# Performance work log

Hardware: AMD Instinct MI355X
Metric: run time of the kernel (lower is better)

The kernel has to match this reference:

```python
import jax, jax.numpy as jnp
import numpy as np

EPS_RHO = 1e-8
EPS_DEN = 1e-9


def _rho_signed_sqrt(x):
    return jnp.sqrt(jax.nn.relu(x) + EPS_RHO) - jnp.sqrt(jax.nn.relu(-x) + EPS_RHO)


def setup_inputs() -> dict:
    key = jax.random.key(0)
    ks = jax.random.split(key, 8)
    B, N, C, A = 2, 512, 1024, 64  # batch, seq, hidden_dim, attn_dim
    s_c = 1.0 / np.sqrt(C)
    s_a = 1.0 / np.sqrt(A)
    return {
        "X": jax.random.normal(ks[0], (B, N, C), jnp.float32),
        "Wq": jax.random.normal(ks[1], (A, C), jnp.float32) * s_c,   # Linear(C->A), no bias
        "Wk": jax.random.normal(ks[2], (A, C), jnp.float32) * s_c,   # Linear(C->A), no bias
        "Wphi": jax.random.normal(ks[3], (A,), jnp.float32) * s_a,   # Linear(A->1), no bias
        "Wy_w": jax.random.normal(ks[4], (C, C), jnp.float32) * s_c, # Linear(C->C)
        "Wy_b": jax.random.normal(ks[5], (C,), jnp.float32) * s_c,
        "We_w": jax.random.normal(ks[6], (C, A), jnp.float32) * s_a, # Linear(A->C)
        "We_b": jax.random.normal(ks[7], (C,), jnp.float32) * s_a,
    }


def reference(X, Wq, Wk, Wphi, Wy_w, Wy_b, We_w, We_b):
    # q, k: (B,N,A); Vy: (B,N,C)
    q = jnp.einsum('bnc,ac->bna', X, Wq)
    k = jnp.einsum('bnc,ac->bna', X, Wk)
    Vy = jnp.einsum('bnc,dc->bnd', X, Wy_w) + Wy_b

    # pairwise features e_ij = relu(rho(q_i + k_j)): (B,N,N,A)
    e = jax.nn.relu(_rho_signed_sqrt(q[:, :, None, :] + k[:, None, :, :]))

    # scores: (B,N,N); stable exp with per-row max (== online-softmax result)
    scores = jnp.einsum('bija,a->bij', e, Wphi)
    m = jnp.max(scores, axis=-1, keepdims=True)
    ex = jnp.exp(scores - m)
    denom = jnp.sum(ex, axis=-1)  # (B,N)

    # part1 = exp_scores @ Vy
    part1 = jnp.einsum('bij,bjc->bic', ex, Vy)
    # part2 = sum_j ex_ij * (We e_ij + be) = We(sum_j ex_ij e_ij) + be * denom  (We is linear)
    Ew = jnp.einsum('bij,bija->bia', ex, e)  # (B,N,A)
    part2 = jnp.einsum('bia,ca->bic', Ew, We_w) + We_b * denom[..., None]

    return (part1 + part2) / (denom[..., None] + EPS_DEN)
```

## Files before the change

kernel.cpp:

```cpp
#include <hip/hip_runtime.h>
#include <math.h>

#define EPS_RHO 1e-8f
#define EPS_DEN 1e-9f

constexpr int Bb = 2;
constexpr int Nn = 512;
constexpr int Cc = 1024;
constexpr int Aa = 64;
constexpr int TOK = Bb * Nn;
constexpr int KGP = 576;

typedef __attribute__((ext_vector_type(8))) short short8;
typedef __attribute__((ext_vector_type(4))) short short4v;
typedef __attribute__((ext_vector_type(4))) float f32x4;

__device__ __forceinline__ float e_fn(float s) {
    const float SQE = 9.9999994e-05f;
    return sqrtf(fmaxf(s, 0.f) + EPS_RHO) - SQE;
}

__device__ __forceinline__ short f2bf(float x) {
    union { float f; unsigned u; } v; v.f = x;
    unsigned r = v.u + 0x7FFFu + ((v.u >> 16) & 1u);
    return (short)(r >> 16);
}

__device__ __forceinline__ unsigned cvt_pk_bf16(float e0, float e1) {
    unsigned d;
    asm("v_cvt_pk_bf16_f32 %0, %1, %2" : "=v"(d) : "v"(e0), "v"(e1));
    return d;
}

constexpr int PREP_N0 = 1024 * 1024;
constexpr int PREP_N1 = 1152 * 1024;
constexpr int PREP_N2 = 2 * 1024 * 64;
constexpr int PREP_TOT = PREP_N0 + PREP_N1 + PREP_N2;

__global__ __launch_bounds__(256) void prep_kernel(
    const float* __restrict__ X, const float* __restrict__ Wy_w,
    const float* __restrict__ Wq, const float* __restrict__ Wk,
    const float* __restrict__ We_w,
    short* __restrict__ Xb, short* __restrict__ Wb, short* __restrict__ Gt)
{
    int g = (blockIdx.x * 256 + threadIdx.x) * 4;
    if (g >= PREP_TOT) return;

    const float* src;
    short* dst;
    if (g < PREP_N0) {
        src = X + g;
        dst = Xb + g;
    } else if (g < PREP_N0 + PREP_N1) {
        int i2 = g - PREP_N0;
        if (i2 < 1048576)       src = Wy_w + i2;
        else if (i2 < 1114112)  src = Wq + (i2 - 1048576);
        else                    src = Wk + (i2 - 1114112);
        dst = Wb + i2;
    } else {
        int i3 = g - PREP_N0 - PREP_N1;
        int b = i3 >> 16;
        int r = i3 & 65535;
        int c = r >> 6, a = r & 63;
        src = We_w + (size_t)c * Aa + a;
        dst = Gt + ((size_t)(b * 1024 + c)) * KGP + 512 + a;
    }
    float4 v = *(const float4*)src;
    short4v o = { f2bf(v.x), f2bf(v.y), f2bf(v.z), f2bf(v.w) };
    *(short4v*)dst = o;
}

__global__ __launch_bounds__(256) void mega_gemm(
    const short* __restrict__ Xb,
    const short* __restrict__ Wb,
    const float* __restrict__ Wy_b,
    short* __restrict__ Gt,
    float* __restrict__ qg,
    float* __restrict__ kTg)
{
    constexpr int K = 1024, BK = 64;
    __shared__ short As[64][72];
    __shared__ short Bs[64][72];

    int tid = threadIdx.x;
    int bm = blockIdx.y * 64;
    int bn = blockIdx.x * 64;
    int row = tid >> 2;
    int kq  = (tid & 3) << 4;

    const short* ag = Xb + (size_t)(bm + row) * K + kq;
    const short* bg = Wb + (size_t)(bn + row) * K + kq;

    short8 ar[2], br[2];
    ar[0] = *(const short8*)ag;       ar[1] = *(const short8*)(ag + 8);
    br[0] = *(const short8*)bg;       br[1] = *(const short8*)(bg + 8);

    int wid = tid >> 6, lane = tid & 63;
    int wm = (wid & 1) * 32, wn = (wid >> 1) * 32;
    int fr = lane & 15, fk = (lane >> 4) * 8;

    f32x4 acc[2][2] = {};

    for (int step = 0; step < K / BK; ++step) {
        __syncthreads();
        *(short8*)&As[row][kq]     = ar[0];
        *(short8*)&As[row][kq + 8] = ar[1];
        *(short8*)&Bs[row][kq]     = br[0];
        *(short8*)&Bs[row][kq + 8] = br[1];
        __syncthreads();

        if (step + 1 < K / BK) {
            const short* ag2 = ag + (size_t)(step + 1) * BK;
            const short* bg2 = bg + (size_t)(step + 1) * BK;
            ar[0] = *(const short8*)ag2;  ar[1] = *(const short8*)(ag2 + 8);
            br[0] = *(const short8*)bg2;  br[1] = *(const short8*)(bg2 + 8);
        }

        #pragma unroll
        for (int kk = 0; kk < 2; ++kk) {
            short8 af[2], bfr[2];
            #pragma unroll
            for (int mi = 0; mi < 2; ++mi)
                af[mi] = *(const short8*)&As[wm + mi * 16 + fr][kk * 32 + fk];
            #pragma unroll
            for (int ni = 0; ni < 2; ++ni)
                bfr[ni] = *(const short8*)&Bs[wn + ni * 16 + fr][kk * 32 + fk];
            #pragma unroll
            for (int mi = 0; mi < 2; ++mi)
                #pragma unroll
                for (int ni = 0; ni < 2; ++ni)
                    acc[mi][ni] = __builtin_amdgcn_mfma_f32_16x16x32_bf16(
                        af[mi], bfr[ni], acc[mi][ni], 0, 0, 0);
        }
    }

    int cr = (lane >> 4) * 4;
    int cc = lane & 15;
    if (bn < 1024) {
        #pragma unroll
        for (int mi = 0; mi < 2; ++mi)
            #pragma unroll
            for (int ni = 0; ni < 2; ++ni) {
                int c = bn + wn + ni * 16 + cc;
                float bv = Wy_b[c];
                #pragma unroll
                for (int r_ = 0; r_ < 4; ++r_) {
                    int t = bm + wm + mi * 16 + cr + r_;
                    int b = t >> 9, j = t & 511;
                    Gt[((size_t)(b * 1024 + c)) * KGP + j] = f2bf(acc[mi][ni][r_] + bv);
                }
            }
    } else if (bn == 1024) {
        #pragma unroll
        for (int mi = 0; mi < 2; ++mi)
            #pragma unroll
            for (int ni = 0; ni < 2; ++ni) {
                int a = wn + ni * 16 + cc;
                #pragma unroll
                for (int r_ = 0; r_ < 4; ++r_) {
                    int t = bm + wm + mi * 16 + cr + r_;
                    qg[(size_t)t * Aa + a] = acc[mi][ni][r_];
                }
            }
    } else {
        #pragma unroll
        for (int mi = 0; mi < 2; ++mi)
            #pragma unroll
            for (int ni = 0; ni < 2; ++ni) {
                int a = wn + ni * 16 + cc;
                #pragma unroll
                for (int r_ = 0; r_ < 4; ++r_) {
                    int t = bm + wm + mi * 16 + cr + r_;
                    int b = t >> 9, j = t & 511;
                    kTg[((size_t)(b * 64 + a)) * 512 + j] = acc[mi][ni][r_];
                }
            }
    }
}

__global__ __launch_bounds__(256) void attn1_fused(
    const float* __restrict__ qg,
    const float* __restrict__ kTg,
    const float* __restrict__ Wphi,
    short* __restrict__ P,
    float* __restrict__ denomg)
{
    __shared__ __align__(16) float qs[Aa];
    __shared__ __align__(16) float wph[Aa];
    __shared__ __align__(16) short E[256][72];
    __shared__ __align__(16) float exs[256];
    __shared__ __align__(16) float red[256];
    __shared__ __align__(16) float ewp[8][Aa];

    int t = blockIdx.x;
    int b = t >> 9;
    int tid = threadIdx.x;

    if (tid < Aa) {
        qs[tid] = qg[(size_t)t * Aa + tid];
        wph[tid] = Wphi[tid];
    }
    __syncthreads();

    const float* kT = kTg + (size_t)b * Aa * 512;

    float dsum = 0.f;
    float ew0 = 0.f, ew1 = 0.f;
    int pa2 = (tid & 31) * 2;
    int pg8 = tid >> 5;

    #pragma unroll
    for (int c = 0; c < 2; ++c) {
        int j = c * 256 + tid;

        float s = 0.f;
        #pragma unroll
        for (int a0 = 0; a0 < Aa; a0 += 8) {
            float e[8];
            #pragma unroll
            for (int u = 0; u < 8; ++u) {
                float kv = kT[(size_t)(a0 + u) * 512 + j];
                e[u] = e_fn(qs[a0 + u] + kv);
                s += wph[a0 + u] * e[u];
            }
            uint4 pk;
            pk.x = cvt_pk_bf16(e[0], e[1]);
            pk.y = cvt_pk_bf16(e[2], e[3]);
            pk.z = cvt_pk_bf16(e[4], e[5]);
            pk.w = cvt_pk_bf16(e[6], e[7]);
            *(uint4*)&E[tid][a0] = pk;
        }
        float ex = expf(s);
        exs[tid] = ex;
        dsum += ex;
        P[(size_t)t * KGP + j] = f2bf(ex);
        __syncthreads();

        #pragma unroll 8
        for (int jj = 0; jj < 32; ++jj) {
            int jr = pg8 * 32 + jj;
            unsigned ue = *(const unsigned*)&E[jr][pa2];
            float e0 = __uint_as_float(ue << 16);
            float e1 = __uint_as_float(ue & 0xFFFF0000u);
            float x = exs[jr];
            ew0 += x * e0;
            ew1 += x * e1;
        }
        __syncthreads();
    }

    red[tid] = dsum;
    __syncthreads();
    for (int off = 128; off > 0; off >>= 1) {
        if (tid < off) red[tid] += red[tid + off];
        __syncthreads();
    }
    if (tid == 0) denomg[t] = red[0];

    ewp[pg8][pa2] = ew0;
    ewp[pg8][pa2 + 1] = ew1;
    __syncthreads();
    if (tid < Aa) {
        float ew = 0.f;
        #pragma unroll
        for (int g = 0; g < 8; ++g) ew += ewp[g][tid];
        P[(size_t)t * KGP + 512 + tid] = f2bf(ew);
    }
}

__global__ __launch_bounds__(256) void attn2_gemm(
    const short* __restrict__ P,
    const short* __restrict__ Gt,
    const float* __restrict__ We_b,
    const float* __restrict__ denomg,
    float* __restrict__ out)
{
    constexpr int BK = 64, NSTEP = KGP / BK;
    __shared__ short As[64][72];
    __shared__ short Bs[64][72];

    int tid = threadIdx.x;
    int bm = blockIdx.y * 64, bn = blockIdx.x * 64;
    int b = bm >> 9;
    int row = tid >> 2;
    int kq  = (tid & 3) << 4;

    const short* ap = P  + (size_t)(bm + row) * KGP + kq;
    const short* bp = Gt + ((size_t)(b * 1024 + bn + row)) * KGP + kq;

    short8 ar[2], br[2];
    ar[0] = *(const short8*)ap;       ar[1] = *(const short8*)(ap + 8);
    br[0] = *(const short8*)bp;       br[1] = *(const short8*)(bp + 8);

    int wid = tid >> 6, lane = tid & 63;
    int wm = (wid & 1) * 32, wn = (wid >> 1) * 32;
    int fr = lane & 15, fk = (lane >> 4) * 8;

    f32x4 acc[2][2] = {};

    for (int step = 0; step < NSTEP; ++step) {
        __syncthreads();
        *(short8*)&As[row][kq]     = ar[0];
        *(short8*)&As[row][kq + 8] = ar[1];
        *(short8*)&Bs[row][kq]     = br[0];
        *(short8*)&Bs[row][kq + 8] = br[1];
        __syncthreads();

        if (step + 1 < NSTEP) {
            const short* ap2 = ap + (size_t)(step + 1) * BK;
            const short* bp2 = bp + (size_t)(step + 1) * BK;
            ar[0] = *(const short8*)ap2;  ar[1] = *(const short8*)(ap2 + 8);
            br[0] = *(const short8*)bp2;  br[1] = *(const short8*)(bp2 + 8);
        }

        #pragma unroll
        for (int kk = 0; kk < 2; ++kk) {
            short8 af[2], bfr[2];
            #pragma unroll
            for (int mi = 0; mi < 2; ++mi)
                af[mi] = *(const short8*)&As[wm + mi * 16 + fr][kk * 32 + fk];
            #pragma unroll
            for (int ni = 0; ni < 2; ++ni)
                bfr[ni] = *(const short8*)&Bs[wn + ni * 16 + fr][kk * 32 + fk];
            #pragma unroll
            for (int mi = 0; mi < 2; ++mi)
                #pragma unroll
                for (int ni = 0; ni < 2; ++ni)
                    acc[mi][ni] = __builtin_amdgcn_mfma_f32_16x16x32_bf16(
                        af[mi], bfr[ni], acc[mi][ni], 0, 0, 0);
        }
    }

    int cr = (lane >> 4) * 4;
    int cc = lane & 15;
    #pragma unroll
    for (int mi = 0; mi < 2; ++mi)
        #pragma unroll
        for (int ni = 0; ni < 2; ++ni) {
            int c = bn + wn + ni * 16 + cc;
            float bv = We_b[c];
            #pragma unroll
            for (int r_ = 0; r_ < 4; ++r_) {
                int t = bm + wm + mi * 16 + cr + r_;
                float dn = denomg[t];
                out[(size_t)t * Cc + c] = (acc[mi][ni][r_] + bv * dn) / (dn + EPS_DEN);
            }
        }
}

extern "C" void kernel_launch(void* const* d_in, const int* in_sizes, int n_in,
                              void* d_out, int out_size, void* d_ws, size_t ws_size,
                              hipStream_t stream)
{
    const float* X    = (const float*)d_in[0];
    const float* Wq   = (const float*)d_in[1];
    const float* Wk   = (const float*)d_in[2];
    const float* Wphi = (const float*)d_in[3];
    const float* Wy_w = (const float*)d_in[4];
    const float* Wy_b = (const float*)d_in[5];
    const float* We_w = (const float*)d_in[6];
    const float* We_b = (const float*)d_in[7];
    float* out = (float*)d_out;

    float* ws = (float*)d_ws;
    float* qg     = ws;
    float* kTg    = qg + (size_t)TOK * Aa;
    float* denomg = kTg + (size_t)TOK * Aa;
    short* Xb     = (short*)(denomg + 1024);
    short* Wb     = Xb + (size_t)1024 * 1024;
    short* Gt     = Wb + (size_t)1152 * 1024;
    short* P      = Gt + (size_t)2 * 1024 * KGP;

    prep_kernel<<<(PREP_TOT / 4 + 255) / 256, 256, 0, stream>>>(
        X, Wy_w, Wq, Wk, We_w, Xb, Wb, Gt);

    dim3 gg(18, 16);
    mega_gemm<<<gg, 256, 0, stream>>>(Xb, Wb, Wy_b, Gt, qg, kTg);

    attn1_fused<<<TOK, 256, 0, stream>>>(qg, kTg, Wphi, P, denomg);

    dim3 g2(16, 16);
    attn2_gemm<<<g2, 256, 0, stream>>>(P, Gt, We_b, denomg, out);
}
```

Before: 121.8 us.

## Replace LDS-tiled GEMMs with split-K direct-load MFMA kernels on smaller tiles

Both bf16 GEMMs now use 32x32 output tiles, with each of the four waves computing a K-slice from operands loaded straight from global memory. The partial results are then summed through shared memory. This removes the LDS staging loop and per-step barriers, and it quadruples the block count so more of the chip's compute units are busy. To make the K splits even, the K dimension of the second GEMM is padded from 576 to 640, and the extra columns are zero-filled in prep and attn1. The trade-offs are redundant global loads with no LDS reuse, less coalesced per-lane loads, and extra zero-padding work.

```diff
diff --git a/kernel.cpp b/kernel.cpp
--- a/kernel.cpp
+++ b/kernel.cpp
@@ -9,7 +9,7 @@
 constexpr int Cc = 1024;
 constexpr int Aa = 64;
 constexpr int TOK = Bb * Nn;
-constexpr int KGP = 576;
+constexpr int KG  = 640;
 
 typedef __attribute__((ext_vector_type(8))) short short8;
 typedef __attribute__((ext_vector_type(4))) short short4v;
@@ -34,7 +34,7 @@
 
 constexpr int PREP_N0 = 1024 * 1024;
 constexpr int PREP_N1 = 1152 * 1024;
-constexpr int PREP_N2 = 2 * 1024 * 64;
+constexpr int PREP_N2 = 2 * 1024 * 128;
 constexpr int PREP_TOT = PREP_N0 + PREP_N1 + PREP_N2;
 
 __global__ __launch_bounds__(256) void prep_kernel(
@@ -46,31 +46,35 @@
     int g = (blockIdx.x * 256 + threadIdx.x) * 4;
     if (g >= PREP_TOT) return;
 
-    const float* src;
-    short* dst;
-    if (g < PREP_N0) {
-        src = X + g;
-        dst = Xb + g;
-    } else if (g < PREP_N0 + PREP_N1) {
-        int i2 = g - PREP_N0;
-        if (i2 < 1048576)       src = Wy_w + i2;
-        else if (i2 < 1114112)  src = Wq + (i2 - 1048576);
-        else                    src = Wk + (i2 - 1114112);
-        dst = Wb + i2;
+    if (g < PREP_N0 + PREP_N1) {
+        const float* src;
+        short* dst;
+        if (g < PREP_N0) { src = X + g; dst = Xb + g; }
+        else {
+            int i2 = g - PREP_N0;
+            if (i2 < 1048576)       src = Wy_w + i2;
+            else if (i2 < 1114112)  src = Wq + (i2 - 1048576);
+            else                    src = Wk + (i2 - 1114112);
+            dst = Wb + i2;
+        }
+        float4 v = *(const float4*)src;
+        short4v o = { f2bf(v.x), f2bf(v.y), f2bf(v.z), f2bf(v.w) };
+        *(short4v*)dst = o;
     } else {
         int i3 = g - PREP_N0 - PREP_N1;
-        int b = i3 >> 16;
-        int r = i3 & 65535;
-        int c = r >> 6, a = r & 63;
-        src = We_w + (size_t)c * Aa + a;
-        dst = Gt + ((size_t)(b * 1024 + c)) * KGP + 512 + a;
-    }
-    float4 v = *(const float4*)src;
-    short4v o = { f2bf(v.x), f2bf(v.y), f2bf(v.z), f2bf(v.w) };
-    *(short4v*)dst = o;
-}
-
-__global__ __launch_bounds__(256) void mega_gemm(
+        int b = i3 >> 17;
+        int r = i3 & 131071;
+        int c = r >> 7, s = r & 127;
+        short4v o = {0, 0, 0, 0};
+        if (s < 64) {
+            float4 v = *(const float4*)(We_w + (size_t)c * Aa + s);
+            o.x = f2bf(v.x); o.y = f2bf(v.y); o.z = f2bf(v.z); o.w = f2bf(v.w);
+        }
+        *(short4v*)(Gt + ((size_t)(b * 1024 + c)) * KG + 512 + s) = o;
+    }
+}
+
+__global__ __launch_bounds__(256) void gemm_mega_direct(
     const short* __restrict__ Xb,
     const short* __restrict__ Wb,
     const float* __restrict__ Wy_b,
@@ -78,103 +82,53 @@
     float* __restrict__ qg,
     float* __restrict__ kTg)
 {
-    constexpr int K = 1024, BK = 64;
-    __shared__ short As[64][72];
-    __shared__ short Bs[64][72];
-
-    int tid = threadIdx.x;
-    int bm = blockIdx.y * 64;
-    int bn = blockIdx.x * 64;
-    int row = tid >> 2;
-    int kq  = (tid & 3) << 4;
-
-    const short* ag = Xb + (size_t)(bm + row) * K + kq;
-    const short* bg = Wb + (size_t)(bn + row) * K + kq;
-
-    short8 ar[2], br[2];
-    ar[0] = *(const short8*)ag;       ar[1] = *(const short8*)(ag + 8);
-    br[0] = *(const short8*)bg;       br[1] = *(const short8*)(bg + 8);
-
-    int wid = tid >> 6, lane = tid & 63;
-    int wm = (wid & 1) * 32, wn = (wid >> 1) * 32;
+    constexpr int K = 1024;
+    int tid = threadIdx.x, wid = tid >> 6, lane = tid & 63;
+    int bm = blockIdx.y * 32, bn = blockIdx.x * 32;
     int fr = lane & 15, fk = (lane >> 4) * 8;
 
+    const short* A0 = Xb + (size_t)(bm + fr) * K + wid * 256 + fk;
+    const short* B0 = Wb + (size_t)(bn + fr) * K + wid * 256 + fk;
+
     f32x4 acc[2][2] = {};
-
-    for (int step = 0; step < K / BK; ++step) {
-        __syncthreads();
-        *(short8*)&As[row][kq]     = ar[0];
-        *(short8*)&As[row][kq + 8] = ar[1];
-        *(short8*)&Bs[row][kq]     = br[0];
-        *(short8*)&Bs[row][kq + 8] = br[1];
-        __syncthreads();
-
-        if (step + 1 < K / BK) {
-            const short* ag2 = ag + (size_t)(step + 1) * BK;
-            const short* bg2 = bg + (size_t)(step + 1) * BK;
-            ar[0] = *(const short8*)ag2;  ar[1] = *(const short8*)(ag2 + 8);
-            br[0] = *(const short8*)bg2;  br[1] = *(const short8*)(bg2 + 8);
-        }
-
+    #pragma unroll 4
+    for (int s = 0; s < 8; ++s) {
+        short8 a0 = *(const short8*)(A0 + s * 32);
+        short8 a1 = *(const short8*)(A0 + 16 * K + s * 32);
+        short8 b0 = *(const short8*)(B0 + s * 32);
+        short8 b1 = *(const short8*)(B0 + 16 * K + s * 32);
+        acc[0][0] = __builtin_amdgcn_mfma_f32_16x16x32_bf16(a0, b0, acc[0][0], 0, 0, 0);
+        acc[0][1] = __builtin_amdgcn_mfma_f32_16x16x32_bf16(a0, b1, acc[0][1], 0, 0, 0);
+        acc[1][0] = __builtin_amdgcn_mfma_f32_16x16x32_bf16(a1, b0, acc[1][0], 0, 0, 0);
+        acc[1][1] = __builtin_amdgcn_mfma_f32_16x16x32_bf16(a1, b1, acc[1][1], 0, 0, 0);
+    }
+
+    __shared__ float red[4][32][34];
+    int cr = (lane >> 4) * 4, cc = lane & 15;
+    #pragma unroll
+    for (int mi = 0; mi < 2; ++mi)
         #pragma unroll
-        for (int kk = 0; kk < 2; ++kk) {
-            short8 af[2], bfr[2];
+        for (int ni = 0; ni < 2; ++ni)
             #pragma unroll
-            for (int mi = 0; mi < 2; ++mi)
-                af[mi] = *(const short8*)&As[wm + mi * 16 + fr][kk * 32 + fk];
-            #pragma unroll
-            for (int ni = 0; ni < 2; ++ni)
-                bfr[ni] = *(const short8*)&Bs[wn + ni * 16 + fr][kk * 32 + fk];
-            #pragma unroll
-            for (int mi = 0; mi < 2; ++mi)
-                #pragma unroll
-                for (int ni = 0; ni < 2; ++ni)
-                    acc[mi][ni] = __builtin_amdgcn_mfma_f32_16x16x32_bf16(
-                        af[mi], bfr[ni], acc[mi][ni], 0, 0, 0);
-        }
-    }
-
-    int cr = (lane >> 4) * 4;
-    int cc = lane & 15;
-    if (bn < 1024) {
-        #pragma unroll
-        for (int mi = 0; mi < 2; ++mi)
-            #pragma unroll
-            for (int ni = 0; ni < 2; ++ni) {
-                int c = bn + wn + ni * 16 + cc;
-                float bv = Wy_b[c];
-                #pragma unroll
-                for (int r_ = 0; r_ < 4; ++r_) {
-                    int t = bm + wm + mi * 16 + cr + r_;
-                    int b = t >> 9, j = t & 511;
-                    Gt[((size_t)(b * 1024 + c)) * KGP + j] = f2bf(acc[mi][ni][r_] + bv);
-                }
-            }
-    } else if (bn == 1024) {
-        #pragma unroll
-        for (int mi = 0; mi < 2; ++mi)
-            #pragma unroll
-            for (int ni = 0; ni < 2; ++ni) {
-                int a = wn + ni * 16 + cc;
-                #pragma unroll
-                for (int r_ = 0; r_ < 4; ++r_) {
-                    int t = bm + wm + mi * 16 + cr + r_;
-                    qg[(size_t)t * Aa + a] = acc[mi][ni][r_];
-                }
-            }
-    } else {
-        #pragma unroll
-        for (int mi = 0; mi < 2; ++mi)
-            #pragma unroll
-            for (int ni = 0; ni < 2; ++ni) {
-                int a = wn + ni * 16 + cc;
-                #pragma unroll
-                for (int r_ = 0; r_ < 4; ++r_) {
-                    int t = bm + wm + mi * 16 + cr + r_;
-                    int b = t >> 9, j = t & 511;
-                    kTg[((size_t)(b * 64 + a)) * 512 + j] = acc[mi][ni][r_];
-                }
-            }
+            for (int r_ = 0; r_ < 4; ++r_)
+                red[wid][mi * 16 + cr + r_][ni * 16 + cc] = acc[mi][ni][r_];
+    __syncthreads();
+
+    int r = tid >> 3, c0 = (tid & 7) * 4;
+    int m = bm + r;
+    int bsel = m >> 9, j = m & 511;
+    #pragma unroll
+    for (int u = 0; u < 4; ++u) {
+        int n = bn + c0 + u;
+        float sum = red[0][r][c0 + u] + red[1][r][c0 + u]
+                  + red[2][r][c0 + u] + red[3][r][c0 + u];
+        if (n < 1024) {
+            Gt[((size_t)(bsel * 1024 + n)) * KG + j] = f2bf(sum + Wy_b[n]);
+        } else if (n < 1088) {
+            qg[(size_t)m * Aa + (n - 1024)] = sum;
+        } else {
+            kTg[((size_t)(bsel * 64 + (n - 1088))) * 512 + j] = sum;
+        }
     }
 }
 
@@ -233,7 +187,7 @@
         float ex = expf(s);
         exs[tid] = ex;
         dsum += ex;
-        P[(size_t)t * KGP + j] = f2bf(ex);
+        P[(size_t)t * KG + j] = f2bf(ex);
         __syncthreads();
 
         #pragma unroll 8
@@ -264,88 +218,65 @@
         float ew = 0.f;
         #pragma unroll
         for (int g = 0; g < 8; ++g) ew += ewp[g][tid];
-        P[(size_t)t * KGP + 512 + tid] = f2bf(ew);
-    }
-}
-
-__global__ __launch_bounds__(256) void attn2_gemm(
+        P[(size_t)t * KG + 512 + tid] = f2bf(ew);
+    } else if (tid < 128) {
+        P[(size_t)t * KG + 576 + (tid - 64)] = 0;
+    }
+}
+
+__global__ __launch_bounds__(256) void gemm_attn2_direct(
     const short* __restrict__ P,
     const short* __restrict__ Gt,
     const float* __restrict__ We_b,
     const float* __restrict__ denomg,
     float* __restrict__ out)
 {
-    constexpr int BK = 64, NSTEP = KGP / BK;
-    __shared__ short As[64][72];
-    __shared__ short Bs[64][72];
-
-    int tid = threadIdx.x;
-    int bm = blockIdx.y * 64, bn = blockIdx.x * 64;
-    int b = bm >> 9;
-    int row = tid >> 2;
-    int kq  = (tid & 3) << 4;
-
-    const short* ap = P  + (size_t)(bm + row) * KGP + kq;
-    const short* bp = Gt + ((size_t)(b * 1024 + bn + row)) * KGP + kq;
-
-    short8 ar[2], br[2];
-    ar[0] = *(const short8*)ap;       ar[1] = *(const short8*)(ap + 8);
-    br[0] = *(const short8*)bp;       br[1] = *(const short8*)(bp + 8);
-
-    int wid = tid >> 6, lane = tid & 63;
-    int wm = (wid & 1) * 32, wn = (wid >> 1) * 32;
+    int tid = threadIdx.x, wid = tid >> 6, lane = tid & 63;
+    int bm = blockIdx.y * 32, bn = blockIdx.x * 32;
+    int bsel = bm >> 9;
     int fr = lane & 15, fk = (lane >> 4) * 8;
 
+    const short* A0 = P + (size_t)(bm + fr) * KG + wid * 160 + fk;
+    const short* B0 = Gt + ((size_t)(bsel * 1024) + bn + fr) * KG + wid * 160 + fk;
+
     f32x4 acc[2][2] = {};
-
-    for (int step = 0; step < NSTEP; ++step) {
-        __syncthreads();
-        *(short8*)&As[row][kq]     = ar[0];
-        *(short8*)&As[row][kq + 8] = ar[1];
-        *(short8*)&Bs[row][kq]     = br[0];
-        *(short8*)&Bs[row][kq + 8] = br[1];
-        __syncthreads();
-
-        if (step + 1 < NSTEP) {
-            const short* ap2 = ap + (size_t)(step + 1) * BK;
-            const short* bp2 = bp + (size_t)(step + 1) * BK;
-            ar[0] = *(const short8*)ap2;  ar[1] = *(const short8*)(ap2 + 8);
-            br[0] = *(const short8*)bp2;  br[1] = *(const short8*)(bp2 + 8);
-        }
-
-        #pragma unroll
-        for (int kk = 0; kk < 2; ++kk) {
-            short8 af[2], bfr[2];
-            #pragma unroll
-            for (int mi = 0; mi < 2; ++mi)
-                af[mi] = *(const short8*)&As[wm + mi * 16 + fr][kk * 32 + fk];
-            #pragma unroll
-            for (int ni = 0; ni < 2; ++ni)
-                bfr[ni] = *(const short8*)&Bs[wn + ni * 16 + fr][kk * 32 + fk];
-            #pragma unroll
-            for (int mi = 0; mi < 2; ++mi)
-                #pragma unroll
-                for (int ni = 0; ni < 2; ++ni)
-                    acc[mi][ni] = __builtin_amdgcn_mfma_f32_16x16x32_bf16(
-                        af[mi], bfr[ni], acc[mi][ni], 0, 0, 0);
-        }
-    }
-
-    int cr = (lane >> 4) * 4;
-    int cc = lane & 15;
+    #pragma unroll
+    for (int s = 0; s < 5; ++s) {
+        short8 a0 = *(const short8*)(A0 + s * 32);
+        short8 a1 = *(const short8*)(A0 + (size_t)16 * KG + s * 32);
+        short8 b0 = *(const short8*)(B0 + s * 32);
+        short8 b1 = *(const short8*)(B0 + (size_t)16 * KG + s * 32);
+        acc[0][0] = __builtin_amdgcn_mfma_f32_16x16x32_bf16(a0, b0, acc[0][0], 0, 0, 0);
+        acc[0][1] = __builtin_amdgcn_mfma_f32_16x16x32_bf16(a0, b1, acc[0][1], 0, 0, 0);
+        acc[1][0] = __builtin_amdgcn_mfma_f32_16x16x32_bf16(a1, b0, acc[1][0], 0, 0, 0);
+        acc[1][1] = __builtin_amdgcn_mfma_f32_16x16x32_bf16(a1, b1, acc[1][1], 0, 0, 0);
+    }
+
+    __shared__ float red[4][32][34];
+    int cr = (lane >> 4) * 4, cc = lane & 15;
     #pragma unroll
     for (int mi = 0; mi < 2; ++mi)
         #pragma unroll
-        for (int ni = 0; ni < 2; ++ni) {
-            int c = bn + wn + ni * 16 + cc;
-            float bv = We_b[c];
+        for (int ni = 0; ni < 2; ++ni)
             #pragma unroll
-            for (int r_ = 0; r_ < 4; ++r_) {
-                int t = bm + wm + mi * 16 + cr + r_;
-                float dn = denomg[t];
-                out[(size_t)t * Cc + c] = (acc[mi][ni][r_] + bv * dn) / (dn + EPS_DEN);
-            }
-        }
+            for (int r_ = 0; r_ < 4; ++r_)
+                red[wid][mi * 16 + cr + r_][ni * 16 + cc] = acc[mi][ni][r_];
+    __syncthreads();
+
+    int r = tid >> 3, c0 = (tid & 7) * 4;
+    int m = bm + r;
+    float dn = denomg[m];
+    float inv = 1.f / (dn + EPS_DEN);
+    float4 o;
+    float* op = &o.x;
+    #pragma unroll
+    for (int u = 0; u < 4; ++u) {
+        int n = bn + c0 + u;
+        float sum = red[0][r][c0 + u] + red[1][r][c0 + u]
+                  + red[2][r][c0 + u] + red[3][r][c0 + u];
+        op[u] = (sum + We_b[n] * dn) * inv;
+    }
+    *(float4*)(out + (size_t)m * Cc + bn + c0) = o;
 }
 
 extern "C" void kernel_launch(void* const* d_in, const int* in_sizes, int n_in,
@@ -369,16 +300,16 @@
     short* Xb     = (short*)(denomg + 1024);
     short* Wb     = Xb + (size_t)1024 * 1024;
     short* Gt     = Wb + (size_t)1152 * 1024;
-    short* P      = Gt + (size_t)2 * 1024 * KGP;
+    short* P      = Gt + (size_t)2 * 1024 * KG;
 
     prep_kernel<<<(PREP_TOT / 4 + 255) / 256, 256, 0, stream>>>(
         X, Wy_w, Wq, Wk, We_w, Xb, Wb, Gt);
 
-    dim3 gg(18, 16);
-    mega_gemm<<<gg, 256, 0, stream>>>(Xb, Wb, Wy_b, Gt, qg, kTg);
+    dim3 gg(36, 32);
+    gemm_mega_direct<<<gg, 256, 0, stream>>>(Xb, Wb, Wy_b, Gt, qg, kTg);
 
     attn1_fused<<<TOK, 256, 0, stream>>>(qg, kTg, Wphi, P, denomg);
 
-    dim3 g2(16, 16);
-    attn2_gemm<<<g2, 256, 0, stream>>>(P, Gt, We_b, denomg, out);
-}
+    dim3 g2(32, 32);
+    gemm_attn2_direct<<<g2, 256, 0, stream>>>(P, Gt, We_b, denomg, out);
+}
```

After: 135.8 us. 1.11x slower.

## Restructure attention pass into per-wave software-pipelined kernel without block barriers

Applied to the files above, without the earlier changes.

Rewrites the pairwise-feature kernel so each wave owns its own slice of keys and shared-memory tiles. Key loads are double-buffered in registers, so the next 16-row load is issued before the current 16 rows are computed. Because the shared tiles are wave-private, the block-wide barriers inside the loop are gone. The denominator is now reduced with wave shuffles instead of a shared-memory tree. The cost is more register pressure (32 floats of buffers), and q and Wphi are now read straight from global or cache rather than staged in shared memory.

```diff
diff --git a/kernel.cpp b/kernel.cpp
--- a/kernel.cpp
+++ b/kernel.cpp
@@ -178,94 +178,120 @@
     }
 }
 
-__global__ __launch_bounds__(256) void attn1_fused(
+#define LOAD16(BUF, AB, JJ)                                     \
+    _Pragma("unroll")                                           \
+    for (int u_ = 0; u_ < 16; ++u_)                             \
+        BUF[u_] = kT[(size_t)((AB) + u_) * 512 + (JJ)];
+
+#define COMP16(BUF, AB)                                         \
+    _Pragma("unroll")                                           \
+    for (int a0_ = 0; a0_ < 16; a0_ += 8) {                     \
+        float e_[8];                                            \
+        _Pragma("unroll")                                       \
+        for (int u_ = 0; u_ < 8; ++u_) {                        \
+            e_[u_] = e_fn(qrow[(AB) + a0_ + u_] + BUF[a0_ + u_]); \
+            s = fmaf(wp[(AB) + a0_ + u_], e_[u_], s);           \
+        }                                                       \
+        uint4 pk_;                                              \
+        pk_.x = cvt_pk_bf16(e_[0], e_[1]);                      \
+        pk_.y = cvt_pk_bf16(e_[2], e_[3]);                      \
+        pk_.z = cvt_pk_bf16(e_[4], e_[5]);                      \
+        pk_.w = cvt_pk_bf16(e_[6], e_[7]);                      \
+        *(uint4*)&E[w][lane][(AB) + a0_] = pk_;                 \
+    }
+
+#define PHASEB()                                                \
+    asm volatile("s_waitcnt lgkmcnt(0)" ::: "memory");          \
+    __builtin_amdgcn_sched_barrier(0);                          \
+    _Pragma("unroll 8")                                         \
+    for (int jj_ = 0; jj_ < 32; ++jj_) {                        \
+        int jr_ = jh * 32 + jj_;                                \
+        float x_ = exsh[w][jr_];                                \
+        unsigned ue_ = *(const unsigned*)&E[w][jr_][pa2];       \
+        ew0 = fmaf(x_, __uint_as_float(ue_ << 16), ew0);        \
+        ew1 = fmaf(x_, __uint_as_float(ue_ & 0xFFFF0000u), ew1);\
+    }                                                           \
+    __builtin_amdgcn_sched_barrier(0);
+
+__global__ __launch_bounds__(256) void attn1_pipe(
     const float* __restrict__ qg,
     const float* __restrict__ kTg,
     const float* __restrict__ Wphi,
     short* __restrict__ P,
     float* __restrict__ denomg)
 {
-    __shared__ __align__(16) float qs[Aa];
-    __shared__ __align__(16) float wph[Aa];
-    __shared__ __align__(16) short E[256][72];
-    __shared__ __align__(16) float exs[256];
-    __shared__ __align__(16) float red[256];
-    __shared__ __align__(16) float ewp[8][Aa];
+    __shared__ __align__(16) short E[4][64][72];
+    __shared__ __align__(16) float exsh[4][64];
+    __shared__ __align__(16) float ewp[4][2][64];
+    __shared__ float dred[4];
 
     int t = blockIdx.x;
     int b = t >> 9;
     int tid = threadIdx.x;
-
-    if (tid < Aa) {
-        qs[tid] = qg[(size_t)t * Aa + tid];
-        wph[tid] = Wphi[tid];
-    }
+    int w = tid >> 6, lane = tid & 63;
+    int pa2 = (lane & 31) * 2;
+    int jh  = lane >> 5;
+
+    const float* kT   = kTg + (size_t)b * Aa * 512;
+    const float* qrow = qg + (size_t)t * Aa;
+    const float* wp   = Wphi;
+
+    int j0 = w * 128 + lane;
+    int j1 = j0 + 64;
+
+    float ka[16], kb[16];
+    float dsum, ew0 = 0.f, ew1 = 0.f;
+
+    LOAD16(ka, 0, j0)
+
+    {
+        float s = 0.f;
+        LOAD16(kb, 16, j0)
+        COMP16(ka, 0)
+        LOAD16(ka, 32, j0)
+        COMP16(kb, 16)
+        LOAD16(kb, 48, j0)
+        COMP16(ka, 32)
+        LOAD16(ka, 0, j1)
+        COMP16(kb, 48)
+        LOAD16(kb, 16, j1)
+        float ex = expf(s);
+        exsh[w][lane] = ex;
+        dsum = ex;
+        P[(size_t)t * KGP + j0] = f2bf(ex);
+        PHASEB()
+    }
+
+    {
+        float s = 0.f;
+        COMP16(ka, 0)
+        LOAD16(ka, 32, j1)
+        COMP16(kb, 16)
+        LOAD16(kb, 48, j1)
+        COMP16(ka, 32)
+        COMP16(kb, 48)
+        float ex = expf(s);
+        exsh[w][lane] = ex;
+        dsum += ex;
+        P[(size_t)t * KGP + j1] = f2bf(ex);
+        PHASEB()
+    }
+
+    ewp[w][jh][pa2]     = ew0;
+    ewp[w][jh][pa2 + 1] = ew1;
+    #pragma unroll
+    for (int m_ = 1; m_ < 64; m_ <<= 1) dsum += __shfl_xor(dsum, m_, 64);
+    if (lane == 0) dred[w] = dsum;
     __syncthreads();
 
-    const float* kT = kTg + (size_t)b * Aa * 512;
-
-    float dsum = 0.f;
-    float ew0 = 0.f, ew1 = 0.f;
-    int pa2 = (tid & 31) * 2;
-    int pg8 = tid >> 5;
-
-    #pragma unroll
-    for (int c = 0; c < 2; ++c) {
-        int j = c * 256 + tid;
-
-        float s = 0.f;
-        #pragma unroll
-        for (int a0 = 0; a0 < Aa; a0 += 8) {
-            float e[8];
-            #pragma unroll
-            for (int u = 0; u < 8; ++u) {
-                float kv = kT[(size_t)(a0 + u) * 512 + j];
-                e[u] = e_fn(qs[a0 + u] + kv);
-                s += wph[a0 + u] * e[u];
-            }
-            uint4 pk;
-            pk.x = cvt_pk_bf16(e[0], e[1]);
-            pk.y = cvt_pk_bf16(e[2], e[3]);
-            pk.z = cvt_pk_bf16(e[4], e[5]);
-            pk.w = cvt_pk_bf16(e[6], e[7]);
-            *(uint4*)&E[tid][a0] = pk;
-        }
-        float ex = expf(s);
-        exs[tid] = ex;
-        dsum += ex;
-        P[(size_t)t * KGP + j] = f2bf(ex);
-        __syncthreads();
-
-        #pragma unroll 8
-        for (int jj = 0; jj < 32; ++jj) {
-            int jr = pg8 * 32 + jj;
-            unsigned ue = *(const unsigned*)&E[jr][pa2];
-            float e0 = __uint_as_float(ue << 16);
-            float e1 = __uint_as_float(ue & 0xFFFF0000u);
-            float x = exs[jr];
-            ew0 += x * e0;
-            ew1 += x * e1;
-        }
-        __syncthreads();
-    }
-
-    red[tid] = dsum;
-    __syncthreads();
-    for (int off = 128; off > 0; off >>= 1) {
-        if (tid < off) red[tid] += red[tid + off];
-        __syncthreads();
-    }
-    if (tid == 0) denomg[t] = red[0];
-
-    ewp[pg8][pa2] = ew0;
-    ewp[pg8][pa2 + 1] = ew1;
-    __syncthreads();
     if (tid < Aa) {
         float ew = 0.f;
         #pragma unroll
-        for (int g = 0; g < 8; ++g) ew += ewp[g][tid];
+        for (int g_ = 0; g_ < 4; ++g_)
+            ew += ewp[g_][0][tid] + ewp[g_][1][tid];
         P[(size_t)t * KGP + 512 + tid] = f2bf(ew);
     }
+    if (tid == 0) denomg[t] = dred[0] + dred[1] + dred[2] + dred[3];
 }
 
 __global__ __launch_bounds__(256) void attn2_gemm(
@@ -377,7 +403,7 @@
     dim3 gg(18, 16);
     mega_gemm<<<gg, 256, 0, stream>>>(Xb, Wb, Wy_b, Gt, qg, kTg);
 
-    attn1_fused<<<TOK, 256, 0, stream>>>(qg, kTg, Wphi, P, denomg);
+    attn1_pipe<<<TOK, 256, 0, stream>>>(qg, kTg, Wphi, P, denomg);
 
     dim3 g2(16, 16);
     attn2_gemm<<<g2, 256, 0, stream>>>(P, Gt, We_b, denomg, out);
```

Result: faster. 116.0 us (-4.8%).

## Rewrite pairwise attention kernel with lane-per-feature layout and DPP wave reductions

Applied to the files above, without the earlier changes.

The pairwise score kernel now assigns one feature dimension per lane and sums the Wphi-weighted features across the wave with DPP steps and readlane, instead of one key per thread with a bf16 staging buffer in LDS. The key projections are stored token-major so each lane reads contiguous feature values. This removes the LDS round trip, the block syncs and the tree reduction, and accumulates Ew in fp32. In exchange it adds a serial chain of cross-lane reductions and a redundant exp on every lane for each key.

```diff
diff --git a/kernel.cpp b/kernel.cpp
--- a/kernel.cpp
+++ b/kernel.cpp
@@ -26,10 +26,20 @@
     return (short)(r >> 16);
 }
 
-__device__ __forceinline__ unsigned cvt_pk_bf16(float e0, float e1) {
-    unsigned d;
-    asm("v_cvt_pk_bf16_f32 %0, %1, %2" : "=v"(d) : "v"(e0), "v"(e1));
-    return d;
+template<int CTRL>
+__device__ __forceinline__ float dpp_add_step(float x) {
+    int y = __builtin_amdgcn_update_dpp(0, __float_as_int(x), CTRL, 0xf, 0xf, true);
+    return x + __int_as_float(y);
+}
+
+__device__ __forceinline__ float wave_sum64(float x) {
+    x = dpp_add_step<0x111>(x);
+    x = dpp_add_step<0x112>(x);
+    x = dpp_add_step<0x114>(x);
+    x = dpp_add_step<0x118>(x);
+    x = dpp_add_step<0x142>(x);
+    x = dpp_add_step<0x143>(x);
+    return __int_as_float(__builtin_amdgcn_readlane(__float_as_int(x), 63));
 }
 
 constexpr int PREP_N0 = 1024 * 1024;
@@ -76,7 +86,7 @@
     const float* __restrict__ Wy_b,
     short* __restrict__ Gt,
     float* __restrict__ qg,
-    float* __restrict__ kTg)
+    float* __restrict__ kg)
 {
     constexpr int K = 1024, BK = 64;
     __shared__ short As[64][72];
@@ -172,100 +182,65 @@
                 for (int r_ = 0; r_ < 4; ++r_) {
                     int t = bm + wm + mi * 16 + cr + r_;
                     int b = t >> 9, j = t & 511;
-                    kTg[((size_t)(b * 64 + a)) * 512 + j] = acc[mi][ni][r_];
+                    kg[((size_t)(b * 512 + j)) * Aa + a] = acc[mi][ni][r_];
                 }
             }
     }
 }
 
-__global__ __launch_bounds__(256) void attn1_fused(
+__global__ __launch_bounds__(256) void attn1_dpp(
     const float* __restrict__ qg,
-    const float* __restrict__ kTg,
+    const float* __restrict__ kg,
     const float* __restrict__ Wphi,
     short* __restrict__ P,
     float* __restrict__ denomg)
 {
-    __shared__ __align__(16) float qs[Aa];
-    __shared__ __align__(16) float wph[Aa];
-    __shared__ __align__(16) short E[256][72];
-    __shared__ __align__(16) float exs[256];
-    __shared__ __align__(16) float red[256];
-    __shared__ __align__(16) float ewp[8][Aa];
-
-    int t = blockIdx.x;
-    int b = t >> 9;
-    int tid = threadIdx.x;
+    __shared__ float ewp[4][64];
+    __shared__ float dred[4];
+
+    int t = blockIdx.x, b = t >> 9;
+    int tid = threadIdx.x, w = tid >> 6, lane = tid & 63;
+
+    const float* krow = kg + ((size_t)(b * 512 + w * 128)) * Aa + lane;
+    float qa = qg[(size_t)t * Aa + lane];
+    float wa = Wphi[lane];
+
+    float kbuf[8];
+    #pragma unroll
+    for (int p = 0; p < 8; ++p) kbuf[p] = krow[(size_t)p * Aa];
+
+    float ew = 0.f, dsum = 0.f;
+
+    #pragma unroll
+    for (int g = 0; g < 2; ++g) {
+        float exreg = 0.f;
+        for (int jb = 0; jb < 8; ++jb) {
+            #pragma unroll
+            for (int u = 0; u < 8; ++u) {
+                int j = g * 64 + jb * 8 + u;
+                float kv = kbuf[u];
+                if (j + 8 < 128)
+                    kbuf[u] = krow[(size_t)(j + 8) * Aa];
+                float e = e_fn(qa + kv);
+                float ss = wave_sum64(wa * e);
+                float ex = exp2f(ss * 1.44269504089f);
+                if (lane == (j & 63)) exreg = ex;
+                dsum += ex;
+                ew = fmaf(ex, e, ew);
+            }
+        }
+        P[(size_t)t * KGP + w * 128 + g * 64 + lane] = f2bf(exreg);
+    }
+
+    ewp[w][lane] = ew;
+    if (lane == 0) dred[w] = dsum;
+    __syncthreads();
 
     if (tid < Aa) {
-        qs[tid] = qg[(size_t)t * Aa + tid];
-        wph[tid] = Wphi[tid];
-    }
-    __syncthreads();
-
-    const float* kT = kTg + (size_t)b * Aa * 512;
-
-    float dsum = 0.f;
-    float ew0 = 0.f, ew1 = 0.f;
-    int pa2 = (tid & 31) * 2;
-    int pg8 = tid >> 5;
-
-    #pragma unroll
-    for (int c = 0; c < 2; ++c) {
-        int j = c * 256 + tid;
-
-        float s = 0.f;
-        #pragma unroll
-        for (int a0 = 0; a0 < Aa; a0 += 8) {
-            float e[8];
-            #pragma unroll
-            for (int u = 0; u < 8; ++u) {
-                float kv = kT[(size_t)(a0 + u) * 512 + j];
-                e[u] = e_fn(qs[a0 + u] + kv);
-                s += wph[a0 + u] * e[u];
-            }
-            uint4 pk;
-            pk.x = cvt_pk_bf16(e[0], e[1]);
-            pk.y = cvt_pk_bf16(e[2], e[3]);
-            pk.z = cvt_pk_bf16(e[4], e[5]);
-            pk.w = cvt_pk_bf16(e[6], e[7]);
-            *(uint4*)&E[tid][a0] = pk;
-        }
-        float ex = expf(s);
-        exs[tid] = ex;
-        dsum += ex;
-        P[(size_t)t * KGP + j] = f2bf(ex);
-        __syncthreads();
-
-        #pragma unroll 8
-        for (int jj = 0; jj < 32; ++jj) {
-            int jr = pg8 * 32 + jj;
-            unsigned ue = *(const unsigned*)&E[jr][pa2];
-            float e0 = __uint_as_float(ue << 16);
-            float e1 = __uint_as_float(ue & 0xFFFF0000u);
-            float x = exs[jr];
-            ew0 += x * e0;
-            ew1 += x * e1;
-        }
-        __syncthreads();
-    }
-
-    red[tid] = dsum;
-    __syncthreads();
-    for (int off = 128; off > 0; off >>= 1) {
-        if (tid < off) red[tid] += red[tid + off];
-        __syncthreads();
-    }
-    if (tid == 0) denomg[t] = red[0];
-
-    ewp[pg8][pa2] = ew0;
-    ewp[pg8][pa2 + 1] = ew1;
-    __syncthreads();
-    if (tid < Aa) {
-        float ew = 0.f;
-        #pragma unroll
-        for (int g = 0; g < 8; ++g) ew += ewp[g][tid];
-        P[(size_t)t * KGP + 512 + tid] = f2bf(ew);
-    }
+        float e4 = ewp[0][tid] + ewp[1][tid] + ewp[2][tid] + ewp[3][tid];
+        P[(size_t)t * KGP + 512 + tid] = f2bf(e4);
+    }
+    if (tid == 0) denomg[t] = dred[0] + dred[1] + dred[2] + dred[3];
 }
 
 __global__ __launch_bounds__(256) void attn2_gemm(
@@ -364,8 +339,8 @@
 
     float* ws = (float*)d_ws;
     float* qg     = ws;
-    float* kTg    = qg + (size_t)TOK * Aa;
-    float* denomg = kTg + (size_t)TOK * Aa;
+    float* kg     = qg + (size_t)TOK * Aa;
+    float* denomg = kg + (size_t)TOK * Aa;
     short* Xb     = (short*)(denomg + 1024);
     short* Wb     = Xb + (size_t)1024 * 1024;
     short* Gt     = Wb + (size_t)1152 * 1024;
@@ -375,9 +350,9 @@
         X, Wy_w, Wq, Wk, We_w, Xb, Wb, Gt);
 
     dim3 gg(18, 16);
-    mega_gemm<<<gg, 256, 0, stream>>>(Xb, Wb, Wy_b, Gt, qg, kTg);
-
-    attn1_fused<<<TOK, 256, 0, stream>>>(qg, kTg, Wphi, P, denomg);
+    mega_gemm<<<gg, 256, 0, stream>>>(Xb, Wb, Wy_b, Gt, qg, kg);
+
+    attn1_dpp<<<TOK, 256, 0, stream>>>(qg, kg, Wphi, P, denomg);
 
     dim3 g2(16, 16);
     attn2_gemm<<<g2, 256, 0, stream>>>(P, Gt, We_b, denomg, out);
```

Result: slower. 131.1 us (+7.6%).
